# Kernel tuning notes

Measured on AMD Instinct MI355X. Metric: run time of the kernel, lower is better.

The kernel has to match this reference:

```python
import jax, jax.numpy as jnp
import numpy as np

HIDDEN = 768
MLP_RATIO = 4
HID_F = HIDDEN * MLP_RATIO          # 3072
NUM_EXPERTS = 6
PART = 192                           # part_features
SHARED = HIDDEN - PART               # 576
B, S = 32, 1024


def setup_inputs() -> dict:
    key = jax.random.key(0)
    ks = jax.random.split(key, 8)
    hidden_state = jax.random.normal(ks[0], (B, S, HIDDEN), dtype=jnp.float32)
    indices = jax.random.randint(ks[1], (B,), 0, NUM_EXPERTS, dtype=jnp.int64)
    sc1 = 1.0 / np.sqrt(HIDDEN)
    sc2 = 1.0 / np.sqrt(HID_F)
    W1 = jax.random.normal(ks[2], (HIDDEN, HID_F), dtype=jnp.float32) * sc1
    b1 = jax.random.normal(ks[3], (HID_F,), dtype=jnp.float32) * sc1
    W2 = jax.random.normal(ks[4], (HID_F, SHARED), dtype=jnp.float32) * sc2
    b2 = jax.random.normal(ks[5], (SHARED,), dtype=jnp.float32) * sc2
    We = jax.random.normal(ks[6], (NUM_EXPERTS, HID_F, PART), dtype=jnp.float32) * sc2
    be = jax.random.normal(ks[7], (NUM_EXPERTS, PART), dtype=jnp.float32) * sc2
    return {"hidden_state": hidden_state, "indices": indices,
            "W1": W1, "b1": b1, "W2": W2, "b2": b2, "We": We, "be": be}


def reference(hidden_state, indices, W1, b1, W2, b2, We, be):
    # fc1 + exact GELU (torch ACT2FN['gelu'])
    h = jnp.einsum('bsd,df->bsf', hidden_state, W1) + b1          # [B,S,HID_F]
    h = jax.nn.gelu(h, approximate=False)
    # shared branch
    shared = jnp.einsum('bsf,fo->bso', h, W2) + b2                # [B,S,SHARED]
    # expert branch: indices select exactly one expert per batch element,
    # so the masked sum over all experts equals gathering the routed expert.
    Wsel = We[indices]                                            # [B,HID_F,PART]
    bsel = be[indices]                                            # [B,PART]
    expert = jnp.einsum('bsf,bfp->bsp', h, Wsel) + bsel[:, None, :]
    return jnp.concatenate([shared, expert], axis=-1)             # [B,S,HIDDEN]
```

## Files before the change

### kernel.cpp

```cpp
#include <hip/hip_runtime.h>
#include <hip/hip_bf16.h>
#include <cstdint>
#include <cstddef>

#define HIDDEN   768
#define HID_F    3072
#define PART     192
#define SHARED_F 576
#define NEXP     6
#define BATCH    32
#define SEQ      1024
#define M_TOK    (BATCH * SEQ)

typedef __bf16 bf16;
typedef __attribute__((ext_vector_type(8))) __bf16 bf16x8;
typedef __attribute__((ext_vector_type(4))) __bf16 bf16x4;
typedef __attribute__((ext_vector_type(4))) float  f32x4;

__device__ __forceinline__ void gl2lds16(const void* g, void* l) {
    __builtin_amdgcn_global_load_lds(
        (const __attribute__((address_space(1))) void*)g,
        (__attribute__((address_space(3))) void*)l,
        16, 0, 0);
}

__device__ __forceinline__ f32x4 mfma16(bf16x8 a, bf16x8 b, f32x4 c) {
    return __builtin_amdgcn_mfma_f32_16x16x32_bf16(a, b, c, 0, 0, 0);
}

#define CFENCE() asm volatile("" ::: "memory")
__device__ __forceinline__ void barrier_raw() {
    CFENCE();
    __builtin_amdgcn_s_barrier();
    CFENCE();
}

__device__ __forceinline__ float gelu_fast(float x) {
    float xs = x * 0.70710678118654752f;
    float ax = __builtin_fabsf(xs);
    float t  = __builtin_amdgcn_rcpf(1.0f + 0.3275911f * ax);
    float p  = t * (0.254829592f +
               t * (-0.284496736f +
               t * (1.421413741f +
               t * (-1.453152027f +
               t * 1.061405429f))));
    float e  = __expf(-xs * xs);
    float er = 1.0f - p * e;
    er = (xs < 0.0f) ? -er : er;
    return 0.5f * x * (1.0f + er);
}

__global__ __launch_bounds__(256) void cvt_f32_bf16(
        const float4* __restrict__ src, bf16x4* __restrict__ dst, int n4) {
    int i      = blockIdx.x * 256 + threadIdx.x;
    int stride = gridDim.x * 256;
    for (; i < n4; i += stride) {
        float4 v = src[i];
        bf16x4 o = { (__bf16)v.x, (__bf16)v.y, (__bf16)v.z, (__bf16)v.w };
        dst[i] = o;
    }
}

__global__ __launch_bounds__(256) void transpose_cvt(
        const float* __restrict__ src, bf16* __restrict__ dst, int K, int N) {
    __shared__ float t[32][33];
    const int n0 = blockIdx.x * 32, k0 = blockIdx.y * 32;
    const int tx = threadIdx.x & 31, ty = threadIdx.x >> 5;
#pragma unroll
    for (int p = 0; p < 4; ++p) {
        int r = ty + p * 8;
        t[r][tx] = src[(size_t)(k0 + r) * N + n0 + tx];
    }
    __syncthreads();
#pragma unroll
    for (int p = 0; p < 4; ++p) {
        int rn = ty + p * 8;
        dst[(size_t)(n0 + rn) * K + k0 + tx] = (bf16)t[tx][rn];
    }
}

__global__ __launch_bounds__(256) void build_wcat(
        const float* __restrict__ W2, const float* __restrict__ We,
        bf16* __restrict__ Wcat) {
    __shared__ float t[32][33];
    const int e  = blockIdx.z;
    const int n0 = blockIdx.x * 32;
    const int k0 = blockIdx.y * 32;
    const int tx = threadIdx.x & 31, ty = threadIdx.x >> 5;
    const float* src;
    int ld, c;
    if (n0 < SHARED_F) { src = W2; ld = SHARED_F; c = n0 + tx; }
    else { src = We + (size_t)e * HID_F * PART; ld = PART; c = n0 + tx - SHARED_F; }
#pragma unroll
    for (int p = 0; p < 4; ++p) {
        int r = ty + p * 8;
        t[r][tx] = src[(size_t)(k0 + r) * ld + c];
    }
    __syncthreads();
    bf16* dst = Wcat + (size_t)e * HIDDEN * HID_F;
#pragma unroll
    for (int p = 0; p < 4; ++p) {
        int rn = ty + p * 8;
        dst[(size_t)(n0 + rn) * HID_F + k0 + tx] = (bf16)t[tx][rn];
    }
}


#define STAGE_A(kt, hm, bb) do {                                          \
    const bf16* g_ = gA + (size_t)((hm) * 128) * LDA + (kt) * 64;         \
    bf16* l_ = lA + ((bb) * 2 + (hm)) * 8192;                             \
    gl2lds16(g_, l_);                                                     \
    gl2lds16(g_ + (size_t)64 * LDA, l_ + 4096);                           \
} while (0)

#define STAGE_B(kt, hm, bb) do {                                          \
    const bf16* g_ = gB + (size_t)((hm) * 128) * LDB + (kt) * 64;         \
    bf16* l_ = lB + ((bb) * 2 + (hm)) * 8192;                             \
    gl2lds16(g_, l_);                                                     \
    gl2lds16(g_ + (size_t)64 * LDB, l_ + 4096);                           \
} while (0)

#define STAGE_B3(kt, nj, bb)                                              \
    gl2lds16(gB + (size_t)((nj) * 64) * LDB + (kt) * 64,                  \
             lB + ((bb) * 3 + (nj)) * 4096)

#define RD_A(dst, qm, bb) do {                                            \
    const bf16* ab_ = fA + ((bb) * 2 + (qm)) * 8192;                      \
    _Pragma("unroll")                                                     \
    for (int mi = 0; mi < 4; ++mi) {                                      \
        dst[mi][0] = *(const bf16x8*)(ab_ + mi * 1024 + pca0);            \
        dst[mi][1] = *(const bf16x8*)(ab_ + mi * 1024 + pca1);            \
    }                                                                     \
} while (0)

#define RD_B(dst, qn, bb) do {                                            \
    const bf16* bb_ = fB + ((bb) * 2 + (qn)) * 8192;                      \
    _Pragma("unroll")                                                     \
    for (int nj = 0; nj < 2; ++nj) {                                      \
        dst[nj][0] = *(const bf16x8*)(bb_ + nj * 1024 + pcb0);            \
        dst[nj][1] = *(const bf16x8*)(bb_ + nj * 1024 + pcb1);            \
    }                                                                     \
} while (0)

#define RD_B3(dst, nj, bb) do {                                           \
    const bf16* b3_ = fB + ((bb) * 3 + (nj)) * 4096;                      \
    dst[0] = *(const bf16x8*)(b3_ + pcb0);                                \
    dst[1] = *(const bf16x8*)(b3_ + pcb1);                                \
} while (0)

#define MFMA16(A_, B_, qm, qn) do {                                       \
    __builtin_amdgcn_s_setprio(1);                                        \
    _Pragma("unroll")                                                     \
    for (int mi = 0; mi < 4; ++mi)                                        \
        _Pragma("unroll")                                                 \
        for (int nj = 0; nj < 2; ++nj) {                                  \
            acc[(qm)*4+mi][(qn)*2+nj] =                                   \
                mfma16(A_[mi][0], B_[nj][0], acc[(qm)*4+mi][(qn)*2+nj]);  \
            acc[(qm)*4+mi][(qn)*2+nj] =                                   \
                mfma16(A_[mi][1], B_[nj][1], acc[(qm)*4+mi][(qn)*2+nj]);  \
        }                                                                 \
    __builtin_amdgcn_s_setprio(0);                                        \
} while (0)

#define MFMA8(A_, B_, qm, nj) do {                                        \
    __builtin_amdgcn_s_setprio(1);                                        \
    _Pragma("unroll")                                                     \
    for (int mi = 0; mi < 4; ++mi) {                                      \
        acc[(qm)*4+mi][nj] =                                              \
            mfma16(A_[mi][0], B_[0], acc[(qm)*4+mi][nj]);                 \
        acc[(qm)*4+mi][nj] =                                              \
            mfma16(A_[mi][1], B_[1], acc[(qm)*4+mi][nj]);                 \
    }                                                                     \
    __builtin_amdgcn_s_setprio(0);                                        \
} while (0)

#define TILE(t, b, bo) do {                                               \
    const int tb1_ = ((t) + 1 < NT) ? (t) + 1 : (t) - 1;                  \
    const int ta2_ = ((t) + 2 < NT) ? (t) + 2 : (t);                      \
     \
    asm volatile("s_waitcnt vmcnt(4)" ::: "memory");                      \
    barrier_raw();                                                        \
    RD_B(bfr1, 1, b);                                                     \
    STAGE_B(tb1_, 1, bo);                                                 \
    MFMA16(afr0, bfr0, 0, 0);                                             \
     \
    RD_A(afr1, 1, b);                                                     \
    STAGE_A(tb1_, 1, bo);                                                 \
    MFMA16(afr0, bfr1, 0, 1);                                             \
     \
    STAGE_A(ta2_, 0, b);                                                  \
    MFMA16(afr1, bfr0, 1, 0);                                             \
     \
    asm volatile("s_waitcnt vmcnt(6)" ::: "memory");                      \
    barrier_raw();                                                        \
    RD_A(afr0, 0, bo);                                                    \
    RD_B(bfr0, 0, bo);                                                    \
    STAGE_B(ta2_, 0, b);                                                  \
    MFMA16(afr1, bfr1, 1, 1);                                             \
} while (0)

__global__ __launch_bounds__(512, 2) void fc1_8ph(
        const bf16*  __restrict__ A,
        const bf16*  __restrict__ Bmat,
        const float* __restrict__ bias1,
        bf16*        __restrict__ Out) {
    constexpr int LDA = HIDDEN, LDB = HIDDEN;
    constexpr int NT  = LDA / 64;
    constexpr int NTILE_N = HID_F / 256;
    constexpr int LDOUT   = HID_F;

    __shared__ alignas(16) bf16 Abuf[2 * 2 * 128 * 64];
    __shared__ alignas(16) bf16 Bbuf[2 * 2 * 128 * 64];

    const int tid  = threadIdx.x;
    const int wave = tid >> 6, lane = tid & 63;
    const int wm = wave >> 2, wn = wave & 3;
    const int lrow = lane & 15, lk8 = (lane >> 4) & 3;

    const int L   = blockIdx.x;
    const int xcd = L & 7;
    const int j   = L >> 3;
    const int jm  = j / NTILE_N;
    const int mt  = xcd * 16 + jm;
    const int nt  = j - jm * NTILE_N;
    const int m0  = mt * 256;
    const int n0  = nt * 256;

    const int srow = tid >> 3;
    const int lch  = (tid & 7) ^ (srow & 7);
    const bf16* gA = A    + (size_t)(m0 + srow) * LDA + lch * 8;
    const bf16* gB = Bmat + (size_t)(n0 + srow) * LDB + lch * 8;
    bf16* lA = Abuf + wave * 512;
    bf16* lB = Bbuf + wave * 512;

    const int rA = wm * 64 + lrow;
    const int rB = wn * 32 + lrow;
    const int pca0 = ((0 + lk8) ^ (rA & 7)) * 8;
    const int pca1 = ((4 + lk8) ^ (rA & 7)) * 8;
    const int pcb0 = ((0 + lk8) ^ (rB & 7)) * 8;
    const int pcb1 = ((4 + lk8) ^ (rB & 7)) * 8;
    const bf16* fA = Abuf + rA * 64;
    const bf16* fB = Bbuf + rB * 64;

    f32x4 acc[8][4] = {};
    bf16x8 afr0[4][2], afr1[4][2], bfr0[2][2], bfr1[2][2];

    STAGE_A(0, 0, 0); STAGE_B(0, 0, 0);
    STAGE_B(0, 1, 0); STAGE_A(0, 1, 0);
    STAGE_A(1, 0, 1); STAGE_B(1, 0, 1);
    asm volatile("s_waitcnt vmcnt(4)" ::: "memory");
    barrier_raw();
    RD_A(afr0, 0, 0);
    RD_B(bfr0, 0, 0);

#pragma unroll 1
    for (int t = 0; t < NT; t += 2) {
        TILE(t,     0, 1);
        TILE(t + 1, 1, 0);
    }

    float bv[4];
#pragma unroll
    for (int nj2 = 0; nj2 < 4; ++nj2) {
        const int col = n0 + (nj2 >> 1) * 128 + wn * 32 + (nj2 & 1) * 16 + lrow;
        bv[nj2] = bias1[col];
    }
#pragma unroll
    for (int mi2 = 0; mi2 < 8; ++mi2) {
        const int row0 = m0 + (mi2 >> 2) * 128 + wm * 64 + (mi2 & 3) * 16 + lk8 * 4;
#pragma unroll
        for (int nj2 = 0; nj2 < 4; ++nj2) {
            const int col = n0 + (nj2 >> 1) * 128 + wn * 32 + (nj2 & 1) * 16 + lrow;
#pragma unroll
            for (int r = 0; r < 4; ++r)
                Out[(size_t)(row0 + r) * LDOUT + col] =
                    (bf16)gelu_fast(acc[mi2][nj2][r] + bv[nj2]);
        }
    }
}

__global__ __launch_bounds__(512, 2) void fc2_moe192(
        const bf16*  __restrict__ A,
        const bf16*  __restrict__ Bmat,
        const float* __restrict__ b2,
        const float* __restrict__ be,
        const int*   __restrict__ idx,
        float*       __restrict__ Out) {
    constexpr int LDA = HID_F, LDB = HID_F;
    constexpr int NT  = LDA / 64;
    constexpr int NTILE_N = HIDDEN / 192;
    constexpr int LDOUT   = HIDDEN;

    __shared__ alignas(16) bf16 Abuf[2 * 2 * 128 * 64];
    __shared__ alignas(16) bf16 Bbuf[2 * 3 * 64 * 64];

    const int tid  = threadIdx.x;
    const int wave = tid >> 6, lane = tid & 63;
    const int wm = wave >> 2, wn = wave & 3;
    const int lrow = lane & 15, lk8 = (lane >> 4) & 3;

    const int L   = blockIdx.x;
    const int xcd = L & 7;
    const int j   = L >> 3;
    const int jm  = j >> 2;
    const int mt  = xcd * 16 + jm;
    const int nt  = j & 3;
    const int m0  = mt * 256;
    const int n0  = nt * 192;

    int e = idx[mt >> 2];
    e = e < 0 ? 0 : (e > NEXP - 1 ? NEXP - 1 : e);
    const bf16* Bt = Bmat + (size_t)e * HIDDEN * HID_F;

    const int srow = tid >> 3;
    const int lch  = (tid & 7) ^ (srow & 7);
    const bf16* gA = A  + (size_t)(m0 + srow) * LDA + lch * 8;
    const bf16* gB = Bt + (size_t)(n0 + srow) * LDB + lch * 8;
    bf16* lA = Abuf + wave * 512;
    bf16* lB = Bbuf + wave * 512;

    const int rA  = wm * 64 + lrow;
    const int rBc = wn * 16 + lrow;
    const int pca0 = ((0 + lk8) ^ (rA & 7)) * 8;
    const int pca1 = ((4 + lk8) ^ (rA & 7)) * 8;
    const int pcb0 = ((0 + lk8) ^ (rBc & 7)) * 8;
    const int pcb1 = ((4 + lk8) ^ (rBc & 7)) * 8;
    const bf16* fA = Abuf + rA * 64;
    const bf16* fB = Bbuf + rBc * 64;

    f32x4 acc[8][3] = {};
    bf16x8 afr0[4][2], afr1[4][2];
    bf16x8 bfrA[2], bfrB[2], bfrC[2];

    STAGE_A(0, 0, 0);
    STAGE_B3(0, 0, 0); STAGE_B3(0, 1, 0); STAGE_B3(0, 2, 0);
    STAGE_A(0, 1, 0);
    STAGE_A(1, 0, 1);
    STAGE_B3(1, 0, 1); STAGE_B3(1, 1, 1);
    asm volatile("s_waitcnt vmcnt(4)" ::: "memory");
    barrier_raw();
    RD_A(afr0, 0, 0);
    RD_B3(bfrA, 0, 0);
    RD_B3(bfrB, 1, 0);

#pragma unroll 1
    for (int t = 0; t < NT; t += 2) {
#pragma unroll
        for (int u = 0; u < 2; ++u) {
            const int tt = t + u;
            const int b  = u, bo = u ^ 1;
            const int tp1 = (tt + 1 < NT) ? tt + 1 : tt - 1;
            const int tp2 = (tt + 2 < NT) ? tt + 2 : tt;
            STAGE_A(tp1, 1, bo);
            asm volatile("s_waitcnt vmcnt(4)" ::: "memory");
            barrier_raw();
            RD_B3(bfrC, 2, b);
            MFMA8(afr0, bfrA, 0, 0);
            MFMA8(afr0, bfrB, 0, 1);
            STAGE_B3(tp1, 2, bo);
            RD_A(afr1, 1, b);
            MFMA8(afr0, bfrC, 0, 2);
            STAGE_A(tp2, 0, b);
            MFMA8(afr1, bfrA, 1, 0);
            MFMA8(afr1, bfrB, 1, 1);
            STAGE_B3(tp2, 0, b); STAGE_B3(tp2, 1, b);
            asm volatile("s_waitcnt vmcnt(4)" ::: "memory");
            barrier_raw();
            RD_A(afr0, 0, bo);
            RD_B3(bfrA, 0, bo);
            RD_B3(bfrB, 1, bo);
            MFMA8(afr1, bfrC, 1, 2);
        }
    }

    float bv[3];
#pragma unroll
    for (int nj = 0; nj < 3; ++nj) {
        const int col = n0 + nj * 64 + wn * 16 + lrow;
        bv[nj] = (col < SHARED_F) ? b2[col] : be[e * PART + col - SHARED_F];
    }
#pragma unroll
    for (int mi2 = 0; mi2 < 8; ++mi2) {
        const int row0 = m0 + (mi2 >> 2) * 128 + wm * 64 + (mi2 & 3) * 16 + lk8 * 4;
#pragma unroll
        for (int nj = 0; nj < 3; ++nj) {
            const int col = n0 + nj * 64 + wn * 16 + lrow;
#pragma unroll
            for (int r = 0; r < 4; ++r)
                Out[(size_t)(row0 + r) * LDOUT + col] = acc[mi2][nj][r] + bv[nj];
        }
    }
}

extern "C" void kernel_launch(void* const* d_in, const int* in_sizes, int n_in,
                              void* d_out, int out_size, void* d_ws, size_t ws_size,
                              hipStream_t stream) {
    const float* hidden = (const float*)d_in[0];
    const int*   idx    = (const int*)d_in[1];
    const float* W1     = (const float*)d_in[2];
    const float* b1     = (const float*)d_in[3];
    const float* W2     = (const float*)d_in[4];
    const float* b2     = (const float*)d_in[5];
    const float* We     = (const float*)d_in[6];
    const float* be     = (const float*)d_in[7];
    float* out = (float*)d_out;

    char* ws = (char*)d_ws;
    bf16* hb   = (bf16*)(ws);
    bf16* h    = (bf16*)(ws + 50331648);
    bf16* W1t  = (bf16*)(ws + 251658240);
    bf16* Wcat = (bf16*)(ws + 256376832);

    cvt_f32_bf16<<<4096, 256, 0, stream>>>(
        (const float4*)hidden, (bf16x4*)hb, (M_TOK * HIDDEN) / 4);
    transpose_cvt<<<dim3(HID_F / 32, HIDDEN / 32), 256, 0, stream>>>(
        W1, W1t, HIDDEN, HID_F);
    build_wcat<<<dim3(HIDDEN / 32, HID_F / 32, NEXP), 256, 0, stream>>>(
        W2, We, Wcat);

    fc1_8ph<<<(M_TOK / 256) * (HID_F / 256), 512, 0, stream>>>(
        hb, W1t, b1, h);

    fc2_moe192<<<(M_TOK / 256) * (HIDDEN / 192), 512, 0, stream>>>(
        h, Wcat, b2, be, idx, out);
}
```

Measured before the change: 546.6 us.

## Fuse all stages into one persistent cooperative kernel with grid syncs

Replaces the five separate launches (input cast, W1 transpose, Wcat build, fc1, fc2) with a single persistent cooperative kernel of 256 blocks. Blocks grid-stride over the conversion work, then over the fc1 and fc2 tiles, with grid.sync between stages. This removes launch overhead and inter-kernel gaps. In exchange, the GEMM phases now run on a fixed 256-block grid at 2 blocks per CU, and the grid-wide barriers add their own synchronisation cost.

```diff
diff --git a/kernel.cpp b/kernel.cpp
--- a/kernel.cpp
+++ b/kernel.cpp
@@ -1,4 +1,5 @@
 #include <hip/hip_runtime.h>
+#include <hip/hip_cooperative_groups.h>
 #include <hip/hip_bf16.h>
 #include <cstdint>
 #include <cstddef>
@@ -11,6 +12,8 @@
 #define BATCH    32
 #define SEQ      1024
 #define M_TOK    (BATCH * SEQ)
+
+namespace cg = cooperative_groups;
 
 typedef __bf16 bf16;
 typedef __attribute__((ext_vector_type(8))) __bf16 bf16x8;
@@ -48,61 +51,6 @@
     float er = 1.0f - p * e;
     er = (xs < 0.0f) ? -er : er;
     return 0.5f * x * (1.0f + er);
-}
-
-__global__ __launch_bounds__(256) void cvt_f32_bf16(
-        const float4* __restrict__ src, bf16x4* __restrict__ dst, int n4) {
-    int i      = blockIdx.x * 256 + threadIdx.x;
-    int stride = gridDim.x * 256;
-    for (; i < n4; i += stride) {
-        float4 v = src[i];
-        bf16x4 o = { (__bf16)v.x, (__bf16)v.y, (__bf16)v.z, (__bf16)v.w };
-        dst[i] = o;
-    }
-}
-
-__global__ __launch_bounds__(256) void transpose_cvt(
-        const float* __restrict__ src, bf16* __restrict__ dst, int K, int N) {
-    __shared__ float t[32][33];
-    const int n0 = blockIdx.x * 32, k0 = blockIdx.y * 32;
-    const int tx = threadIdx.x & 31, ty = threadIdx.x >> 5;
-#pragma unroll
-    for (int p = 0; p < 4; ++p) {
-        int r = ty + p * 8;
-        t[r][tx] = src[(size_t)(k0 + r) * N + n0 + tx];
-    }
-    __syncthreads();
-#pragma unroll
-    for (int p = 0; p < 4; ++p) {
-        int rn = ty + p * 8;
-        dst[(size_t)(n0 + rn) * K + k0 + tx] = (bf16)t[tx][rn];
-    }
-}
-
-__global__ __launch_bounds__(256) void build_wcat(
-        const float* __restrict__ W2, const float* __restrict__ We,
-        bf16* __restrict__ Wcat) {
-    __shared__ float t[32][33];
-    const int e  = blockIdx.z;
-    const int n0 = blockIdx.x * 32;
-    const int k0 = blockIdx.y * 32;
-    const int tx = threadIdx.x & 31, ty = threadIdx.x >> 5;
-    const float* src;
-    int ld, c;
-    if (n0 < SHARED_F) { src = W2; ld = SHARED_F; c = n0 + tx; }
-    else { src = We + (size_t)e * HID_F * PART; ld = PART; c = n0 + tx - SHARED_F; }
-#pragma unroll
-    for (int p = 0; p < 4; ++p) {
-        int r = ty + p * 8;
-        t[r][tx] = src[(size_t)(k0 + r) * ld + c];
-    }
-    __syncthreads();
-    bf16* dst = Wcat + (size_t)e * HIDDEN * HID_F;
-#pragma unroll
-    for (int p = 0; p < 4; ++p) {
-        int rn = ty + p * 8;
-        dst[(size_t)(n0 + rn) * HID_F + k0 + tx] = (bf16)t[tx][rn];
-    }
 }
 
 
@@ -199,195 +147,261 @@
     MFMA16(afr1, bfr1, 1, 1);                                             \
 } while (0)
 
-__global__ __launch_bounds__(512, 2) void fc1_8ph(
-        const bf16*  __restrict__ A,
-        const bf16*  __restrict__ Bmat,
-        const float* __restrict__ bias1,
-        bf16*        __restrict__ Out) {
-    constexpr int LDA = HIDDEN, LDB = HIDDEN;
-    constexpr int NT  = LDA / 64;
-    constexpr int NTILE_N = HID_F / 256;
-    constexpr int LDOUT   = HID_F;
-
+__global__ void __launch_bounds__(512, 2) fused_moe(
+        const float* __restrict__ hidden, const int* __restrict__ idx,
+        const float* __restrict__ W1, const float* __restrict__ b1,
+        const float* __restrict__ W2, const float* __restrict__ b2,
+        const float* __restrict__ We, const float* __restrict__ be,
+        float* __restrict__ out,
+        bf16* __restrict__ hb, bf16* __restrict__ h,
+        bf16* __restrict__ W1t, bf16* __restrict__ Wcat) {
     __shared__ alignas(16) bf16 Abuf[2 * 2 * 128 * 64];
     __shared__ alignas(16) bf16 Bbuf[2 * 2 * 128 * 64];
 
     const int tid  = threadIdx.x;
+    const int bid  = blockIdx.x;
     const int wave = tid >> 6, lane = tid & 63;
     const int wm = wave >> 2, wn = wave & 3;
     const int lrow = lane & 15, lk8 = (lane >> 4) & 3;
-
-    const int L   = blockIdx.x;
-    const int xcd = L & 7;
-    const int j   = L >> 3;
-    const int jm  = j / NTILE_N;
-    const int mt  = xcd * 16 + jm;
-    const int nt  = j - jm * NTILE_N;
-    const int m0  = mt * 256;
-    const int n0  = nt * 256;
-
-    const int srow = tid >> 3;
-    const int lch  = (tid & 7) ^ (srow & 7);
-    const bf16* gA = A    + (size_t)(m0 + srow) * LDA + lch * 8;
-    const bf16* gB = Bmat + (size_t)(n0 + srow) * LDB + lch * 8;
-    bf16* lA = Abuf + wave * 512;
-    bf16* lB = Bbuf + wave * 512;
-
-    const int rA = wm * 64 + lrow;
-    const int rB = wn * 32 + lrow;
-    const int pca0 = ((0 + lk8) ^ (rA & 7)) * 8;
-    const int pca1 = ((4 + lk8) ^ (rA & 7)) * 8;
-    const int pcb0 = ((0 + lk8) ^ (rB & 7)) * 8;
-    const int pcb1 = ((4 + lk8) ^ (rB & 7)) * 8;
-    const bf16* fA = Abuf + rA * 64;
-    const bf16* fB = Bbuf + rB * 64;
-
-    f32x4 acc[8][4] = {};
-    bf16x8 afr0[4][2], afr1[4][2], bfr0[2][2], bfr1[2][2];
-
-    STAGE_A(0, 0, 0); STAGE_B(0, 0, 0);
-    STAGE_B(0, 1, 0); STAGE_A(0, 1, 0);
-    STAGE_A(1, 0, 1); STAGE_B(1, 0, 1);
-    asm volatile("s_waitcnt vmcnt(4)" ::: "memory");
-    barrier_raw();
-    RD_A(afr0, 0, 0);
-    RD_B(bfr0, 0, 0);
-
-#pragma unroll 1
-    for (int t = 0; t < NT; t += 2) {
-        TILE(t,     0, 1);
-        TILE(t + 1, 1, 0);
-    }
-
-    float bv[4];
-#pragma unroll
-    for (int nj2 = 0; nj2 < 4; ++nj2) {
-        const int col = n0 + (nj2 >> 1) * 128 + wn * 32 + (nj2 & 1) * 16 + lrow;
-        bv[nj2] = bias1[col];
-    }
-#pragma unroll
-    for (int mi2 = 0; mi2 < 8; ++mi2) {
-        const int row0 = m0 + (mi2 >> 2) * 128 + wm * 64 + (mi2 & 3) * 16 + lk8 * 4;
-#pragma unroll
-        for (int nj2 = 0; nj2 < 4; ++nj2) {
-            const int col = n0 + (nj2 >> 1) * 128 + wn * 32 + (nj2 & 1) * 16 + lrow;
-#pragma unroll
-            for (int r = 0; r < 4; ++r)
-                Out[(size_t)(row0 + r) * LDOUT + col] =
-                    (bf16)gelu_fast(acc[mi2][nj2][r] + bv[nj2]);
+    const int xcd  = bid & 7;
+    const int bx   = bid >> 3;
+
+    cg::grid_group grid = cg::this_grid();
+
+    {
+        const float4* src4 = (const float4*)hidden;
+        bf16x4* dst4 = (bf16x4*)hb;
+        int i = bid * 512 + tid;
+#pragma unroll 4
+        for (int it = 0; it < 48; ++it, i += 131072) {
+            float4 v = src4[i];
+            bf16x4 o = { (__bf16)v.x, (__bf16)v.y, (__bf16)v.z, (__bf16)v.w };
+            dst4[i] = o;
         }
     }
-}
-
-__global__ __launch_bounds__(512, 2) void fc2_moe192(
-        const bf16*  __restrict__ A,
-        const bf16*  __restrict__ Bmat,
-        const float* __restrict__ b2,
-        const float* __restrict__ be,
-        const int*   __restrict__ idx,
-        float*       __restrict__ Out) {
-    constexpr int LDA = HID_F, LDB = HID_F;
-    constexpr int NT  = LDA / 64;
-    constexpr int NTILE_N = HIDDEN / 192;
-    constexpr int LDOUT   = HIDDEN;
-
-    __shared__ alignas(16) bf16 Abuf[2 * 2 * 128 * 64];
-    __shared__ alignas(16) bf16 Bbuf[2 * 3 * 64 * 64];
-
-    const int tid  = threadIdx.x;
-    const int wave = tid >> 6, lane = tid & 63;
-    const int wm = wave >> 2, wn = wave & 3;
-    const int lrow = lane & 15, lk8 = (lane >> 4) & 3;
-
-    const int L   = blockIdx.x;
-    const int xcd = L & 7;
-    const int j   = L >> 3;
-    const int jm  = j >> 2;
-    const int mt  = xcd * 16 + jm;
-    const int nt  = j & 3;
-    const int m0  = mt * 256;
-    const int n0  = nt * 192;
-
-    int e = idx[mt >> 2];
-    e = e < 0 ? 0 : (e > NEXP - 1 ? NEXP - 1 : e);
-    const bf16* Bt = Bmat + (size_t)e * HIDDEN * HID_F;
-
-    const int srow = tid >> 3;
-    const int lch  = (tid & 7) ^ (srow & 7);
-    const bf16* gA = A  + (size_t)(m0 + srow) * LDA + lch * 8;
-    const bf16* gB = Bt + (size_t)(n0 + srow) * LDB + lch * 8;
-    bf16* lA = Abuf + wave * 512;
-    bf16* lB = Bbuf + wave * 512;
-
-    const int rA  = wm * 64 + lrow;
-    const int rBc = wn * 16 + lrow;
-    const int pca0 = ((0 + lk8) ^ (rA & 7)) * 8;
-    const int pca1 = ((4 + lk8) ^ (rA & 7)) * 8;
-    const int pcb0 = ((0 + lk8) ^ (rBc & 7)) * 8;
-    const int pcb1 = ((4 + lk8) ^ (rBc & 7)) * 8;
-    const bf16* fA = Abuf + rA * 64;
-    const bf16* fB = Bbuf + rBc * 64;
-
-    f32x4 acc[8][3] = {};
-    bf16x8 afr0[4][2], afr1[4][2];
-    bf16x8 bfrA[2], bfrB[2], bfrC[2];
-
-    STAGE_A(0, 0, 0);
-    STAGE_B3(0, 0, 0); STAGE_B3(0, 1, 0); STAGE_B3(0, 2, 0);
-    STAGE_A(0, 1, 0);
-    STAGE_A(1, 0, 1);
-    STAGE_B3(1, 0, 1); STAGE_B3(1, 1, 1);
-    asm volatile("s_waitcnt vmcnt(4)" ::: "memory");
-    barrier_raw();
-    RD_A(afr0, 0, 0);
-    RD_B3(bfrA, 0, 0);
-    RD_B3(bfrB, 1, 0);
-
-#pragma unroll 1
-    for (int t = 0; t < NT; t += 2) {
-#pragma unroll
-        for (int u = 0; u < 2; ++u) {
-            const int tt = t + u;
-            const int b  = u, bo = u ^ 1;
-            const int tp1 = (tt + 1 < NT) ? tt + 1 : tt - 1;
-            const int tp2 = (tt + 2 < NT) ? tt + 2 : tt;
-            STAGE_A(tp1, 1, bo);
+    {
+        float (*tb)[32][33] = (float(*)[32][33])Abuf;
+        const int u  = tid >> 8;
+        const int unit = bid * 2 + u;
+        const int lt = tid & 255;
+        const int tx = lt & 31, ty = lt >> 5;
+
+        for (int it = 0; it < 5; ++it) {
+            const int tl = unit + it * 512;
+            const bool act = tl < 2304;
+            const int n0 = (tl % 96) * 32;
+            const int k0 = (tl / 96) * 32;
+            if (act) {
+#pragma unroll
+                for (int p = 0; p < 4; ++p) {
+                    int r = ty + p * 8;
+                    tb[u][r][tx] = W1[(size_t)(k0 + r) * HID_F + n0 + tx];
+                }
+            }
+            __syncthreads();
+            if (act) {
+#pragma unroll
+                for (int p = 0; p < 4; ++p) {
+                    int rn = ty + p * 8;
+                    W1t[(size_t)(n0 + rn) * HIDDEN + k0 + tx] = (bf16)tb[u][tx][rn];
+                }
+            }
+            __syncthreads();
+        }
+
+        for (int it = 0; it < 27; ++it) {
+            const int tl = unit + it * 512;
+            const int n0 = (tl % 24) * 32;
+            const int k0 = ((tl / 24) % 96) * 32;
+            const int e  = tl / (24 * 96);
+            const float* src; int ld, c;
+            if (n0 < SHARED_F) { src = W2; ld = SHARED_F; c = n0 + tx; }
+            else { src = We + (size_t)e * HID_F * PART; ld = PART; c = n0 + tx - SHARED_F; }
+#pragma unroll
+            for (int p = 0; p < 4; ++p) {
+                int r = ty + p * 8;
+                tb[u][r][tx] = src[(size_t)(k0 + r) * ld + c];
+            }
+            __syncthreads();
+            bf16* dst = Wcat + (size_t)e * HIDDEN * HID_F;
+#pragma unroll
+            for (int p = 0; p < 4; ++p) {
+                int rn = ty + p * 8;
+                dst[(size_t)(n0 + rn) * HID_F + k0 + tx] = (bf16)tb[u][tx][rn];
+            }
+            __syncthreads();
+        }
+    }
+
+    __threadfence();
+    grid.sync();
+
+    {
+        constexpr int LDA = HIDDEN, LDB = HIDDEN;
+        constexpr int NT  = LDA / 64;
+        constexpr int LDOUT = HID_F;
+
+        const int rA = wm * 64 + lrow;
+        const int rB = wn * 32 + lrow;
+        const int pca0 = ((0 + lk8) ^ (rA & 7)) * 8;
+        const int pca1 = ((4 + lk8) ^ (rA & 7)) * 8;
+        const int pcb0 = ((0 + lk8) ^ (rB & 7)) * 8;
+        const int pcb1 = ((4 + lk8) ^ (rB & 7)) * 8;
+        const bf16* fA = Abuf + rA * 64;
+        const bf16* fB = Bbuf + rB * 64;
+        bf16* lA = Abuf + wave * 512;
+        bf16* lB = Bbuf + wave * 512;
+        const int srow = tid >> 3;
+        const int lch  = (tid & 7) ^ (srow & 7);
+
+        for (int it = 0; it < 6; ++it) {
+            const int j  = bx * 6 + it;
+            const int jm = j / 12;
+            const int nt = j - jm * 12;
+            const int mt = xcd * 16 + jm;
+            const int m0 = mt * 256;
+            const int n0 = nt * 256;
+
+            const bf16* gA = hb  + (size_t)(m0 + srow) * LDA + lch * 8;
+            const bf16* gB = W1t + (size_t)(n0 + srow) * LDB + lch * 8;
+
+            f32x4 acc[8][4] = {};
+            bf16x8 afr0[4][2], afr1[4][2], bfr0[2][2], bfr1[2][2];
+
+            STAGE_A(0, 0, 0); STAGE_B(0, 0, 0);
+            STAGE_B(0, 1, 0); STAGE_A(0, 1, 0);
+            STAGE_A(1, 0, 1); STAGE_B(1, 0, 1);
             asm volatile("s_waitcnt vmcnt(4)" ::: "memory");
             barrier_raw();
-            RD_B3(bfrC, 2, b);
-            MFMA8(afr0, bfrA, 0, 0);
-            MFMA8(afr0, bfrB, 0, 1);
-            STAGE_B3(tp1, 2, bo);
-            RD_A(afr1, 1, b);
-            MFMA8(afr0, bfrC, 0, 2);
-            STAGE_A(tp2, 0, b);
-            MFMA8(afr1, bfrA, 1, 0);
-            MFMA8(afr1, bfrB, 1, 1);
-            STAGE_B3(tp2, 0, b); STAGE_B3(tp2, 1, b);
+            RD_A(afr0, 0, 0);
+            RD_B(bfr0, 0, 0);
+
+#pragma unroll 1
+            for (int t = 0; t < NT; t += 2) {
+                TILE(t,     0, 1);
+                TILE(t + 1, 1, 0);
+            }
+
+            float bv[4];
+#pragma unroll
+            for (int nj2 = 0; nj2 < 4; ++nj2) {
+                const int col = n0 + (nj2 >> 1) * 128 + wn * 32 + (nj2 & 1) * 16 + lrow;
+                bv[nj2] = b1[col];
+            }
+#pragma unroll
+            for (int mi2 = 0; mi2 < 8; ++mi2) {
+                const int row0 = m0 + (mi2 >> 2) * 128 + wm * 64 + (mi2 & 3) * 16 + lk8 * 4;
+#pragma unroll
+                for (int nj2 = 0; nj2 < 4; ++nj2) {
+                    const int col = n0 + (nj2 >> 1) * 128 + wn * 32 + (nj2 & 1) * 16 + lrow;
+#pragma unroll
+                    for (int r = 0; r < 4; ++r)
+                        h[(size_t)(row0 + r) * LDOUT + col] =
+                            (bf16)gelu_fast(acc[mi2][nj2][r] + bv[nj2]);
+                }
+            }
+            barrier_raw();
+        }
+    }
+
+    __threadfence();
+    grid.sync();
+
+    {
+        constexpr int LDA = HID_F, LDB = HID_F;
+        constexpr int NT  = LDA / 64;
+        constexpr int LDOUT = HIDDEN;
+
+        const int rA  = wm * 64 + lrow;
+        const int rBc = wn * 16 + lrow;
+        const int pca0 = ((0 + lk8) ^ (rA & 7)) * 8;
+        const int pca1 = ((4 + lk8) ^ (rA & 7)) * 8;
+        const int pcb0 = ((0 + lk8) ^ (rBc & 7)) * 8;
+        const int pcb1 = ((4 + lk8) ^ (rBc & 7)) * 8;
+        const bf16* fA = Abuf + rA * 64;
+        const bf16* fB = Bbuf + rBc * 64;
+        bf16* lA = Abuf + wave * 512;
+        bf16* lB = Bbuf + wave * 512;
+        const int srow = tid >> 3;
+        const int lch  = (tid & 7) ^ (srow & 7);
+
+        for (int it = 0; it < 2; ++it) {
+            const int j2 = bx * 2 + it;
+            const int mt = xcd * 16 + (j2 >> 2);
+            const int nt = j2 & 3;
+            const int m0 = mt * 256;
+            const int n0 = nt * 192;
+
+            int e = idx[mt >> 2];
+            e = e < 0 ? 0 : (e > NEXP - 1 ? NEXP - 1 : e);
+            const bf16* Bt = Wcat + (size_t)e * HIDDEN * HID_F;
+
+            const bf16* gA = h  + (size_t)(m0 + srow) * LDA + lch * 8;
+            const bf16* gB = Bt + (size_t)(n0 + srow) * LDB + lch * 8;
+
+            f32x4 acc[8][3] = {};
+            bf16x8 afr0[4][2], afr1[4][2];
+            bf16x8 bfrA[2], bfrB[2], bfrC[2];
+
+            STAGE_A(0, 0, 0);
+            STAGE_B3(0, 0, 0); STAGE_B3(0, 1, 0); STAGE_B3(0, 2, 0);
+            STAGE_A(0, 1, 0);
+            STAGE_A(1, 0, 1);
+            STAGE_B3(1, 0, 1); STAGE_B3(1, 1, 1);
             asm volatile("s_waitcnt vmcnt(4)" ::: "memory");
             barrier_raw();
-            RD_A(afr0, 0, bo);
-            RD_B3(bfrA, 0, bo);
-            RD_B3(bfrB, 1, bo);
-            MFMA8(afr1, bfrC, 1, 2);
-        }
-    }
-
-    float bv[3];
-#pragma unroll
-    for (int nj = 0; nj < 3; ++nj) {
-        const int col = n0 + nj * 64 + wn * 16 + lrow;
-        bv[nj] = (col < SHARED_F) ? b2[col] : be[e * PART + col - SHARED_F];
-    }
-#pragma unroll
-    for (int mi2 = 0; mi2 < 8; ++mi2) {
-        const int row0 = m0 + (mi2 >> 2) * 128 + wm * 64 + (mi2 & 3) * 16 + lk8 * 4;
-#pragma unroll
-        for (int nj = 0; nj < 3; ++nj) {
-            const int col = n0 + nj * 64 + wn * 16 + lrow;
-#pragma unroll
-            for (int r = 0; r < 4; ++r)
-                Out[(size_t)(row0 + r) * LDOUT + col] = acc[mi2][nj][r] + bv[nj];
+            RD_A(afr0, 0, 0);
+            RD_B3(bfrA, 0, 0);
+            RD_B3(bfrB, 1, 0);
+
+#pragma unroll 1
+            for (int t = 0; t < NT; t += 2) {
+#pragma unroll
+                for (int u = 0; u < 2; ++u) {
+                    const int tt = t + u;
+                    const int b  = u, bo = u ^ 1;
+                    const int tp1 = (tt + 1 < NT) ? tt + 1 : tt - 1;
+                    const int tp2 = (tt + 2 < NT) ? tt + 2 : tt;
+                    STAGE_A(tp1, 1, bo);
+                    asm volatile("s_waitcnt vmcnt(4)" ::: "memory");
+                    barrier_raw();
+                    RD_B3(bfrC, 2, b);
+                    MFMA8(afr0, bfrA, 0, 0);
+                    MFMA8(afr0, bfrB, 0, 1);
+                    STAGE_B3(tp1, 2, bo);
+                    RD_A(afr1, 1, b);
+                    MFMA8(afr0, bfrC, 0, 2);
+                    STAGE_A(tp2, 0, b);
+                    MFMA8(afr1, bfrA, 1, 0);
+                    MFMA8(afr1, bfrB, 1, 1);
+                    STAGE_B3(tp2, 0, b); STAGE_B3(tp2, 1, b);
+                    asm volatile("s_waitcnt vmcnt(4)" ::: "memory");
+                    barrier_raw();
+                    RD_A(afr0, 0, bo);
+                    RD_B3(bfrA, 0, bo);
+                    RD_B3(bfrB, 1, bo);
+                    MFMA8(afr1, bfrC, 1, 2);
+                }
+            }
+
+            float bv[3];
+#pragma unroll
+            for (int nj = 0; nj < 3; ++nj) {
+                const int col = n0 + nj * 64 + wn * 16 + lrow;
+                bv[nj] = (col < SHARED_F) ? b2[col] : be[e * PART + col - SHARED_F];
+            }
+#pragma unroll
+            for (int mi2 = 0; mi2 < 8; ++mi2) {
+                const int row0 = m0 + (mi2 >> 2) * 128 + wm * 64 + (mi2 & 3) * 16 + lk8 * 4;
+#pragma unroll
+                for (int nj = 0; nj < 3; ++nj) {
+                    const int col = n0 + nj * 64 + wn * 16 + lrow;
+#pragma unroll
+                    for (int r = 0; r < 4; ++r)
+                        out[(size_t)(row0 + r) * LDOUT + col] = acc[mi2][nj][r] + bv[nj];
+                }
+            }
+            barrier_raw();
         }
     }
 }
@@ -411,16 +425,11 @@
     bf16* W1t  = (bf16*)(ws + 251658240);
     bf16* Wcat = (bf16*)(ws + 256376832);
 
-    cvt_f32_bf16<<<4096, 256, 0, stream>>>(
-        (const float4*)hidden, (bf16x4*)hb, (M_TOK * HIDDEN) / 4);
-    transpose_cvt<<<dim3(HID_F / 32, HIDDEN / 32), 256, 0, stream>>>(
-        W1, W1t, HIDDEN, HID_F);
-    build_wcat<<<dim3(HIDDEN / 32, HID_F / 32, NEXP), 256, 0, stream>>>(
-        W2, We, Wcat);
-
-    fc1_8ph<<<(M_TOK / 256) * (HID_F / 256), 512, 0, stream>>>(
-        hb, W1t, b1, h);
-
-    fc2_moe192<<<(M_TOK / 256) * (HIDDEN / 192), 512, 0, stream>>>(
-        h, Wcat, b2, be, idx, out);
-}
+    void* args[] = {
+        (void*)&hidden, (void*)&idx, (void*)&W1, (void*)&b1,
+        (void*)&W2, (void*)&b2, (void*)&We, (void*)&be,
+        (void*)&out, (void*)&hb, (void*)&h, (void*)&W1t, (void*)&Wcat
+    };
+    hipLaunchCooperativeKernel((const void*)fused_moe,
+                               dim3(256), dim3(512), args, 0, stream);
+}
```

Result: slower. 774.6 us (+41.7%).
